# Kernel tuning notes

Measured on AMD Instinct MI355X. Metric: run time of the kernel, lower is better.

Reference implementation:

```python
import jax, jax.numpy as jnp
import numpy as np

EMB = 2048
HEADS = 16


def setup_inputs() -> dict:
    key = jax.random.key(0)
    k_x, k_wqkv, k_bqkv, k_wo, k_bo = jax.random.split(key, 5)
    B, S, E = 2, 2048, EMB
    x = jax.random.normal(k_x, (B, S, E), dtype=jnp.float32)
    # nn.Linear weights stored as (in, out) for x @ W + b convention
    W_qkv = jax.random.normal(k_wqkv, (E, 3 * E), dtype=jnp.float32) * 0.02
    b_qkv = jax.random.normal(k_bqkv, (3 * E,), dtype=jnp.float32) * 0.02
    W_out = jax.random.normal(k_wo, (E, E), dtype=jnp.float32) * 0.02
    b_out = jax.random.normal(k_bo, (E,), dtype=jnp.float32) * 0.02
    return {"x": x, "W_qkv": W_qkv, "b_qkv": b_qkv, "W_out": W_out, "b_out": b_out}


def reference(x, W_qkv, b_qkv, W_out, b_out):
    B, S, E = x.shape
    H = HEADS
    dh = E // H
    # QKV projection: (B,S,3E)
    qkv = x @ W_qkv + b_qkv
    # Faithful to torch: reshape (B,S,H,3*dh) THEN split -> interleaved per-head q/k/v
    qkv = qkv.reshape(B, S, H, 3 * dh).transpose(0, 2, 1, 3)  # (B,H,S,3*dh)
    q, k, v = jnp.split(qkv, 3, axis=-1)  # each (B,H,S,dh)
    q = q / jnp.asarray(dh, q.dtype) ** 0.5
    scores = jnp.einsum('bhqd,bhkd->bhqk', q, k)  # (B,H,S,S)
    weights = jax.nn.softmax(scores, axis=-1)
    attn = jnp.einsum('bhqk,bhkd->bhqd', weights, v)  # (B,H,S,dh)
    attn = attn.transpose(0, 2, 1, 3).reshape(B, S, E)
    return attn @ W_out + b_out
```

## Files before the change

kernel.cpp:

```cpp
#include <hip/hip_runtime.h>
#include <type_traits>
#include <utility>

#define DI __device__ __forceinline__

typedef unsigned short u16;
typedef float f32x4 __attribute__((ext_vector_type(4)));
typedef float f32x16 __attribute__((ext_vector_type(16)));
typedef short s16x8 __attribute__((ext_vector_type(8)));
typedef __bf16 bf16x8 __attribute__((ext_vector_type(8)));

template <typename V, typename = void>
struct mfma_ok : std::false_type {};
template <typename V>
struct mfma_ok<V, std::void_t<decltype(__builtin_amdgcn_mfma_f32_16x16x32_bf16(
    std::declval<V>(), std::declval<V>(), std::declval<f32x4>(), 0, 0, 0))>>
    : std::true_type {};
using frag_t = std::conditional_t<mfma_ok<bf16x8>::value, bf16x8, s16x8>;

union U128 {
  int4 i;
  frag_t f;
  u16 s[8];
};

DI f32x4 mfma16(const U128& a, const U128& b, f32x4 c) {
  return __builtin_amdgcn_mfma_f32_16x16x32_bf16(a.f, b.f, c, 0, 0, 0);
}
DI f32x16 mfma32(const U128& a, const U128& b, f32x16 c) {
  return __builtin_amdgcn_mfma_f32_32x32x16_bf16(a.f, b.f, c, 0, 0, 0);
}

DI u16 f2b(float x) {
  union { float f; unsigned u; } v; v.f = x;
  unsigned r = v.u + 0x7FFFu + ((v.u >> 16) & 1u);
  return (u16)(r >> 16);
}

#if __has_builtin(__builtin_amdgcn_exp2f)
#define EXP2F __builtin_amdgcn_exp2f
#else
#define EXP2F exp2f
#endif

typedef __attribute__((address_space(1))) void gas_t;
typedef __attribute__((address_space(3))) void las_t;
DI void gll16(const void* g, void* l) {
  __builtin_amdgcn_global_load_lds((gas_t*)g, (las_t*)l, 16, 0, 0);
}

__global__ __launch_bounds__(256) void k_conv_bf16(const float* __restrict__ in,
                                                   u16* __restrict__ out, int n4) {
  int i = blockIdx.x * 256 + threadIdx.x;
  if (i >= n4) return;
  float4 v = ((const float4*)in)[i];
  ushort4 o;
  o.x = f2b(v.x); o.y = f2b(v.y); o.z = f2b(v.z); o.w = f2b(v.w);
  ((ushort4*)out)[i] = o;
}

__global__ __launch_bounds__(256) void k_transpose_f2b(const float* __restrict__ in,
                                                       u16* __restrict__ out,
                                                       int R, int C) {
  __shared__ __attribute__((aligned(16))) u16 Tb[64][68];
  int t = threadIdx.x;
  long r0 = (long)blockIdx.y * 64, c0 = (long)blockIdx.x * 64;
  int cq = (t & 15) * 4, rr = t >> 4;
#pragma unroll
  for (int it = 0; it < 4; ++it) {
    int r = rr + it * 16;
    float4 v = *(const float4*)(in + (r0 + r) * C + c0 + cq);
    Tb[r][cq + 0] = f2b(v.x); Tb[r][cq + 1] = f2b(v.y);
    Tb[r][cq + 2] = f2b(v.z); Tb[r][cq + 3] = f2b(v.w);
  }
  __syncthreads();
#pragma unroll
  for (int it = 0; it < 2; ++it) {
    int ci = it * 256 + t;
    int cc = ci >> 3, ch = ci & 7, rb = ch * 8;
    unsigned p0 = Tb[rb + 0][cc] | ((unsigned)Tb[rb + 1][cc] << 16);
    unsigned p1 = Tb[rb + 2][cc] | ((unsigned)Tb[rb + 3][cc] << 16);
    unsigned p2 = Tb[rb + 4][cc] | ((unsigned)Tb[rb + 5][cc] << 16);
    unsigned p3 = Tb[rb + 6][cc] | ((unsigned)Tb[rb + 7][cc] << 16);
    *(int4*)(out + (c0 + cc) * R + r0 + rb) = make_int4(p0, p1, p2, p3);
  }
}

template <bool BF16OUT>
__global__ __launch_bounds__(256, 4) void k_gemm_bt(const u16* __restrict__ A,
                                                    const u16* __restrict__ Bt,
                                                    const float* __restrict__ bias,
                                                    void* __restrict__ Cout,
                                                    int M, int N, int K) {
  __shared__ __attribute__((aligned(16))) u16 As[128 * 64];
  __shared__ __attribute__((aligned(16))) u16 Bs[128 * 64];
  int t = threadIdx.x;
  int lane = t & 63, w = t >> 6, quad = lane >> 4, l15 = lane & 15;
  long m0 = (long)blockIdx.y * 128, n0 = (long)blockIdx.x * 128;
  int wr = (w >> 1) * 64, wc = (w & 1) * 64;
  int sw = l15 & 7;
  f32x4 acc[4][4] = {};
  for (int k0 = 0; k0 < K; k0 += 64) {
    __syncthreads();
#pragma unroll
    for (int it = 0; it < 4; ++it) {
      int ci = it * 256 + t;
      int row = ci >> 3, cl = (ci & 7) ^ (row & 7);
      gll16(A + (m0 + row) * K + k0 + cl * 8, As + ci * 8);
      gll16(Bt + (n0 + row) * K + k0 + cl * 8, Bs + ci * 8);
    }
    __syncthreads();
#pragma unroll
    for (int kk = 0; kk < 2; ++kk) {
      U128 a[4], b[4];
#pragma unroll
      for (int i = 0; i < 4; ++i)
        a[i].i = *(const int4*)(As + (wr + i * 16 + l15) * 64 + (((kk * 4 + quad) ^ sw) << 3));
#pragma unroll
      for (int j = 0; j < 4; ++j)
        b[j].i = *(const int4*)(Bs + (wc + j * 16 + l15) * 64 + (((kk * 4 + quad) ^ sw) << 3));
#pragma unroll
      for (int i = 0; i < 4; ++i)
#pragma unroll
        for (int j = 0; j < 4; ++j)
          acc[i][j] = mfma16(a[i], b[j], acc[i][j]);
    }
  }
  float bj[4];
#pragma unroll
  for (int j = 0; j < 4; ++j) bj[j] = bias[n0 + wc + j * 16 + l15];
#pragma unroll
  for (int i = 0; i < 4; ++i) {
#pragma unroll
    for (int r = 0; r < 4; ++r) {
      long row = m0 + wr + i * 16 + quad * 4 + r;
#pragma unroll
      for (int j = 0; j < 4; ++j) {
        long col = n0 + wc + j * 16 + l15;
        float v = acc[i][j][r] + bj[j];
        if (BF16OUT) {
          unsigned pb = f2b(v);
          unsigned other = __shfl_xor(pb, 1);
          if (!(l15 & 1))
            ((unsigned*)Cout)[(row * N + col) >> 1] = pb | (other << 16);
        } else {
          ((float*)Cout)[row * N + col] = v;
        }
      }
    }
  }
}

__global__ __launch_bounds__(256) void k_extract_kvt(const u16* __restrict__ qkv,
                                                     u16* __restrict__ kb,
                                                     u16* __restrict__ vt) {
  __shared__ __attribute__((aligned(16))) u16 Vb[64][136];
  int t = threadIdx.x;
  int s0 = blockIdx.x * 64;
  int bh = blockIdx.y, b = bh >> 4, h = bh & 15;
  long rowbase = (long)b * 2048 + s0;
  long krowout = (long)bh * 2048 + s0;
#pragma unroll
  for (int it = 0; it < 4; ++it) {
    int ci = it * 256 + t;
    int s = ci >> 4, ch = ci & 15;
    int4 v = *(const int4*)(qkv + (rowbase + s) * 6144 + h * 384 + 128 + ch * 8);
    *(int4*)(kb + (krowout + s) * 128 + ch * 8) = v;
  }
#pragma unroll
  for (int it = 0; it < 4; ++it) {
    int ci = it * 256 + t;
    int s = ci >> 4, ch = ci & 15;
    int4 v = *(const int4*)(qkv + (rowbase + s) * 6144 + h * 384 + 256 + ch * 8);
    *(int4*)(&Vb[s][ch * 8]) = v;
  }
  __syncthreads();
  long outbase = (long)bh * 128 * 2048 + s0;
#pragma unroll
  for (int it = 0; it < 4; ++it) {
    int ci = it * 256 + t;
    int d = ci >> 3, ch = ci & 7, sb = ch * 8;
    unsigned p0 = Vb[sb + 0][d] | ((unsigned)Vb[sb + 1][d] << 16);
    unsigned p1 = Vb[sb + 2][d] | ((unsigned)Vb[sb + 3][d] << 16);
    unsigned p2 = Vb[sb + 4][d] | ((unsigned)Vb[sb + 5][d] << 16);
    unsigned p3 = Vb[sb + 6][d] | ((unsigned)Vb[sb + 7][d] << 16);
    *(int4*)(vt + outbase + (long)d * 2048 + sb) = make_int4(p0, p1, p2, p3);
  }
}

__global__ __launch_bounds__(256, 2) void k_flash(const u16* __restrict__ qkv,
                                                  const u16* __restrict__ kb,
                                                  const u16* __restrict__ vt,
                                                  u16* __restrict__ attn) {
  __shared__ __attribute__((aligned(16))) u16 Ks[64 * 128];
  __shared__ __attribute__((aligned(16))) u16 Vts[128 * 64];
  int t = threadIdx.x;
  int lane = t & 63, w = t >> 6, l31 = lane & 31, h = lane >> 5;
  int q0 = blockIdx.x * 128 + w * 32;
  int bh = blockIdx.y, b = bh >> 4, hd = bh & 15;

  const u16* qbase = qkv + ((long)b * 2048 + q0 + l31) * 6144 + hd * 384;
  U128 qf[8];
#pragma unroll
  for (int dht = 0; dht < 8; ++dht)
    qf[dht].i = *(const int4*)(qbase + dht * 16 + h * 8);

  f32x16 O[4] = {};
  float lsum = 0.f;
  const float CEXP = 0.08838834764831845f * 1.4426950408889634f;
  const u16* kbh = kb + (long)bh * 2048 * 128;
  long vbase = (long)bh * 128 * 2048;

  for (int k0 = 0; k0 < 2048; k0 += 64) {
    __syncthreads();
#pragma unroll
    for (int it = 0; it < 4; ++it) {
      int ci = it * 256 + t;
      int key = ci >> 4, cp = ci & 15, cl = cp ^ (key & 7);
      gll16(kbh + (k0 + key) * 128 + cl * 8, Ks + ci * 8);
    }
#pragma unroll
    for (int it = 0; it < 4; ++it) {
      int ci = it * 256 + t;
      int d = ci >> 3, cp = ci & 7, cl = cp ^ (d & 7);
      gll16(vt + vbase + (long)d * 2048 + k0 + cl * 8, Vts + ci * 8);
    }
    __syncthreads();

    f32x16 St[2] = {};
#pragma unroll
    for (int kb2 = 0; kb2 < 2; ++kb2) {
      int row = kb2 * 32 + l31, sw = row & 7;
      const u16* kr = Ks + row * 128;
#pragma unroll
      for (int dht = 0; dht < 8; ++dht) {
        U128 kf;
        kf.i = *(const int4*)(kr + (((dht * 2 + h) ^ sw) << 3));
        St[kb2] = mfma32(kf, qf[dht], St[kb2]);
      }
    }

    float pk[2][16];
#pragma unroll
    for (int kb2 = 0; kb2 < 2; ++kb2)
#pragma unroll
      for (int r = 0; r < 16; ++r) {
        float p = EXP2F(St[kb2][r] * CEXP);
        pk[kb2][r] = p;
        lsum += p;
      }

    U128 pf[4];
#pragma unroll
    for (int kb2 = 0; kb2 < 2; ++kb2)
#pragma unroll
      for (int g = 0; g < 2; ++g) {
        float tmp[4], recv[4], lo[4], hi[4];
#pragma unroll
        for (int i = 0; i < 4; ++i)
          tmp[i] = h ? pk[kb2][g * 8 + i] : pk[kb2][g * 8 + 4 + i];
#pragma unroll
        for (int i = 0; i < 4; ++i) recv[i] = __shfl_xor(tmp[i], 32);
#pragma unroll
        for (int i = 0; i < 4; ++i) {
          lo[i] = h ? recv[i] : pk[kb2][g * 8 + i];
          hi[i] = h ? pk[kb2][g * 8 + 4 + i] : recv[i];
        }
        unsigned w0 = f2b(lo[0]) | ((unsigned)f2b(lo[1]) << 16);
        unsigned w1 = f2b(lo[2]) | ((unsigned)f2b(lo[3]) << 16);
        unsigned w2 = f2b(hi[0]) | ((unsigned)f2b(hi[1]) << 16);
        unsigned w3 = f2b(hi[2]) | ((unsigned)f2b(hi[3]) << 16);
        pf[kb2 * 2 + g].i = make_int4(w0, w1, w2, w3);
      }

#pragma unroll
    for (int kt = 0; kt < 4; ++kt)
#pragma unroll
      for (int dht = 0; dht < 4; ++dht) {
        int vrow = dht * 32 + l31, vsw = vrow & 7;
        U128 vf;
        vf.i = *(const int4*)(Vts + vrow * 64 + (((kt * 2 + h) ^ vsw) << 3));
        O[dht] = mfma32(vf, pf[kt], O[dht]);
      }
  }

  float ltot = lsum + __shfl_xor(lsum, 32);
  float inv = 1.f / ltot;
  long orow = (long)b * 2048 + q0 + l31;
  u16* ob = attn + orow * 2048 + hd * 128;
#pragma unroll
  for (int dht = 0; dht < 4; ++dht)
#pragma unroll
    for (int g = 0; g < 4; ++g) {
      int dh = dht * 32 + g * 8 + h * 4;
      float v0 = O[dht][4 * g + 0] * inv, v1 = O[dht][4 * g + 1] * inv;
      float v2 = O[dht][4 * g + 2] * inv, v3 = O[dht][4 * g + 3] * inv;
      uint2 pkd;
      pkd.x = f2b(v0) | ((unsigned)f2b(v1) << 16);
      pkd.y = f2b(v2) | ((unsigned)f2b(v3) << 16);
      *(uint2*)(ob + dh) = pkd;
    }
}

extern "C" void kernel_launch(void* const* d_in, const int* in_sizes, int n_in,
                              void* d_out, int out_size, void* d_ws, size_t ws_size,
                              hipStream_t stream) {
  const float* x    = (const float*)d_in[0];
  const float* Wqkv = (const float*)d_in[1];
  const float* bqkv = (const float*)d_in[2];
  const float* Wout = (const float*)d_in[3];
  const float* bout = (const float*)d_in[4];
  float* out = (float*)d_out;
  char* ws = (char*)d_ws;

  if (ws_size < 75497472u) return;

  u16* xb    = (u16*)d_out;
  u16* wqkvt = (u16*)(ws);
  u16* qkvb  = (u16*)(ws + 25165824);
  u16* vtb   = (u16*)d_out;
  u16* kbuf  = (u16*)((char*)d_out + 16777216);
  u16* woutt = (u16*)(ws);
  u16* attnb = (u16*)(ws + 8388608);

  k_conv_bf16<<<8192, 256, 0, stream>>>(x, xb, 2097152);
  k_transpose_f2b<<<dim3(96, 32), 256, 0, stream>>>(Wqkv, wqkvt, 2048, 6144);
  k_gemm_bt<true><<<dim3(48, 32), 256, 0, stream>>>(xb, wqkvt, bqkv, qkvb, 4096, 6144, 2048);
  k_extract_kvt<<<dim3(32, 32), 256, 0, stream>>>(qkvb, kbuf, vtb);
  k_transpose_f2b<<<dim3(32, 32), 256, 0, stream>>>(Wout, woutt, 2048, 2048);
  k_flash<<<dim3(16, 32), 256, 0, stream>>>(qkvb, kbuf, vtb, attnb);
  k_gemm_bt<false><<<dim3(16, 32), 256, 0, stream>>>(attnb, woutt, bout, out, 4096, 2048, 2048);
}
```

Before: 398.0 us.

## Split flash attention keys across warp pairs and vectorize fp32 GEMM stores

The flash kernel now gives each block 64 queries instead of 128. Each pair of warps handles half of the key range (split-K), and the partial outputs and row sums are combined through shared memory at the end. This doubles the grid to 1024 blocks and raises the occupancy hint to 3, to fill more CUs on a launch that was only 512 blocks. The cost is more K/V loads per query and an extra shared-memory reduction. Separately, the fp32 output GEMM epilogue pairs adjacent columns with a lane shuffle and writes them as 8-byte stores.

```diff
diff --git a/kernel.cpp b/kernel.cpp
--- a/kernel.cpp
+++ b/kernel.cpp
@@ -144,7 +144,12 @@
           if (!(l15 & 1))
             ((unsigned*)Cout)[(row * N + col) >> 1] = pb | (other << 16);
         } else {
-          ((float*)Cout)[row * N + col] = v;
+          unsigned bits = __float_as_uint(v);
+          unsigned other = __shfl_xor(bits, 1);
+          if (!(l15 & 1)) {
+            uint2 pr; pr.x = bits; pr.y = other;
+            *(uint2*)((float*)Cout + row * N + col) = pr;
+          }
         }
       }
     }
@@ -188,15 +193,20 @@
   }
 }
 
-__global__ __launch_bounds__(256, 2) void k_flash(const u16* __restrict__ qkv,
+__global__ __launch_bounds__(256, 3) void k_flash(const u16* __restrict__ qkv,
                                                   const u16* __restrict__ kb,
                                                   const u16* __restrict__ vt,
                                                   u16* __restrict__ attn) {
-  __shared__ __attribute__((aligned(16))) u16 Ks[64 * 128];
-  __shared__ __attribute__((aligned(16))) u16 Vts[128 * 64];
+  __shared__ __attribute__((aligned(16))) char smraw[49152];
+  u16* Ks = (u16*)smraw;
+  u16* Vts = (u16*)(smraw + 16384);
+  float* Om = (float*)smraw;
+  float* Lm = (float*)(smraw + 33024);
+
   int t = threadIdx.x;
   int lane = t & 63, w = t >> 6, l31 = lane & 31, h = lane >> 5;
-  int q0 = blockIdx.x * 128 + w * 32;
+  int qg = w & 1, kg = w >> 1, tl = t & 127;
+  int q0 = blockIdx.x * 64 + qg * 32;
   int bh = blockIdx.y, b = bh >> 4, hd = bh & 15;
 
   const u16* qbase = qkv + ((long)b * 2048 + q0 + l31) * 6144 + hd * 384;
@@ -210,96 +220,113 @@
   const float CEXP = 0.08838834764831845f * 1.4426950408889634f;
   const u16* kbh = kb + (long)bh * 2048 * 128;
   long vbase = (long)bh * 128 * 2048;
-
-  for (int k0 = 0; k0 < 2048; k0 += 64) {
+  u16* KsH = Ks + kg * 4096;
+  u16* VtsH = Vts + kg * 8192;
+  int kstart = kg * 1024;
+  int sw15 = l31 & 15;
+
+  for (int tile = 0; tile < 32; ++tile) {
+    int k0 = kstart + tile * 32;
     __syncthreads();
 #pragma unroll
     for (int it = 0; it < 4; ++it) {
-      int ci = it * 256 + t;
-      int key = ci >> 4, cp = ci & 15, cl = cp ^ (key & 7);
-      gll16(kbh + (k0 + key) * 128 + cl * 8, Ks + ci * 8);
-    }
-#pragma unroll
-    for (int it = 0; it < 4; ++it) {
-      int ci = it * 256 + t;
-      int d = ci >> 3, cp = ci & 7, cl = cp ^ (d & 7);
-      gll16(vt + vbase + (long)d * 2048 + k0 + cl * 8, Vts + ci * 8);
+      int ci = it * 128 + tl;
+      int key = ci >> 4, cp = ci & 15, cl = cp ^ (key & 15);
+      gll16(kbh + (long)(k0 + key) * 128 + cl * 8, KsH + ci * 8);
+    }
+    if (!(tile & 1)) {
+#pragma unroll
+      for (int it = 0; it < 8; ++it) {
+        int ci = it * 128 + tl;
+        int d = ci >> 3, cp = ci & 7, cl = cp ^ (d & 7);
+        gll16(vt + vbase + (long)d * 2048 + k0 + cl * 8, VtsH + ci * 8);
+      }
     }
     __syncthreads();
 
-    f32x16 St[2] = {};
-#pragma unroll
-    for (int kb2 = 0; kb2 < 2; ++kb2) {
-      int row = kb2 * 32 + l31, sw = row & 7;
-      const u16* kr = Ks + row * 128;
-#pragma unroll
-      for (int dht = 0; dht < 8; ++dht) {
-        U128 kf;
-        kf.i = *(const int4*)(kr + (((dht * 2 + h) ^ sw) << 3));
-        St[kb2] = mfma32(kf, qf[dht], St[kb2]);
-      }
-    }
-
-    float pk[2][16];
-#pragma unroll
-    for (int kb2 = 0; kb2 < 2; ++kb2)
+    f32x16 St = {};
+#pragma unroll
+    for (int dht = 0; dht < 8; ++dht) {
+      U128 kf;
+      kf.i = *(const int4*)(KsH + l31 * 128 + (((dht * 2 + h) ^ sw15) << 3));
+      St = mfma32(kf, qf[dht], St);
+    }
+
+    float pk[16];
+#pragma unroll
+    for (int r = 0; r < 16; ++r) {
+      float p = EXP2F(St[r] * CEXP);
+      pk[r] = p;
+      lsum += p;
+    }
+
+    U128 pf[2];
+#pragma unroll
+    for (int g = 0; g < 2; ++g) {
+      float tmp[4], recv[4], lo[4], hi[4];
+#pragma unroll
+      for (int i = 0; i < 4; ++i)
+        tmp[i] = h ? pk[g * 8 + i] : pk[g * 8 + 4 + i];
+#pragma unroll
+      for (int i = 0; i < 4; ++i) recv[i] = __shfl_xor(tmp[i], 32);
+#pragma unroll
+      for (int i = 0; i < 4; ++i) {
+        lo[i] = h ? recv[i] : pk[g * 8 + i];
+        hi[i] = h ? pk[g * 8 + 4 + i] : recv[i];
+      }
+      unsigned w0 = f2b(lo[0]) | ((unsigned)f2b(lo[1]) << 16);
+      unsigned w1 = f2b(lo[2]) | ((unsigned)f2b(lo[3]) << 16);
+      unsigned w2 = f2b(hi[0]) | ((unsigned)f2b(hi[1]) << 16);
+      unsigned w3 = f2b(hi[2]) | ((unsigned)f2b(hi[3]) << 16);
+      pf[g].i = make_int4(w0, w1, w2, w3);
+    }
+
+    int koff = (tile & 1) * 4;
+#pragma unroll
+    for (int kt = 0; kt < 2; ++kt)
+#pragma unroll
+      for (int dht = 0; dht < 4; ++dht) {
+        int vrow = dht * 32 + l31;
+        U128 vf;
+        vf.i = *(const int4*)(VtsH + vrow * 64 + (((koff + kt * 2 + h) ^ (vrow & 7)) << 3));
+        O[dht] = mfma32(vf, pf[kt], O[dht]);
+      }
+  }
+
+  float lhalf = lsum + __shfl_xor(lsum, 32);
+  __syncthreads();
+  if (kg == 1) {
+    if (lane < 32) Lm[qg * 32 + l31] = lhalf;
+#pragma unroll
+    for (int dht = 0; dht < 4; ++dht)
 #pragma unroll
       for (int r = 0; r < 16; ++r) {
-        float p = EXP2F(St[kb2][r] * CEXP);
-        pk[kb2][r] = p;
-        lsum += p;
-      }
-
-    U128 pf[4];
-#pragma unroll
-    for (int kb2 = 0; kb2 < 2; ++kb2)
-#pragma unroll
-      for (int g = 0; g < 2; ++g) {
-        float tmp[4], recv[4], lo[4], hi[4];
-#pragma unroll
-        for (int i = 0; i < 4; ++i)
-          tmp[i] = h ? pk[kb2][g * 8 + i] : pk[kb2][g * 8 + 4 + i];
-#pragma unroll
-        for (int i = 0; i < 4; ++i) recv[i] = __shfl_xor(tmp[i], 32);
-#pragma unroll
-        for (int i = 0; i < 4; ++i) {
-          lo[i] = h ? recv[i] : pk[kb2][g * 8 + i];
-          hi[i] = h ? pk[kb2][g * 8 + 4 + i] : recv[i];
-        }
-        unsigned w0 = f2b(lo[0]) | ((unsigned)f2b(lo[1]) << 16);
-        unsigned w1 = f2b(lo[2]) | ((unsigned)f2b(lo[3]) << 16);
-        unsigned w2 = f2b(hi[0]) | ((unsigned)f2b(hi[1]) << 16);
-        unsigned w3 = f2b(hi[2]) | ((unsigned)f2b(hi[3]) << 16);
-        pf[kb2 * 2 + g].i = make_int4(w0, w1, w2, w3);
-      }
-
-#pragma unroll
-    for (int kt = 0; kt < 4; ++kt)
-#pragma unroll
-      for (int dht = 0; dht < 4; ++dht) {
-        int vrow = dht * 32 + l31, vsw = vrow & 7;
-        U128 vf;
-        vf.i = *(const int4*)(Vts + vrow * 64 + (((kt * 2 + h) ^ vsw) << 3));
-        O[dht] = mfma32(vf, pf[kt], O[dht]);
-      }
-  }
-
-  float ltot = lsum + __shfl_xor(lsum, 32);
-  float inv = 1.f / ltot;
-  long orow = (long)b * 2048 + q0 + l31;
-  u16* ob = attn + orow * 2048 + hd * 128;
-#pragma unroll
-  for (int dht = 0; dht < 4; ++dht)
-#pragma unroll
-    for (int g = 0; g < 4; ++g) {
-      int dh = dht * 32 + g * 8 + h * 4;
-      float v0 = O[dht][4 * g + 0] * inv, v1 = O[dht][4 * g + 1] * inv;
-      float v2 = O[dht][4 * g + 2] * inv, v3 = O[dht][4 * g + 3] * inv;
-      uint2 pkd;
-      pkd.x = f2b(v0) | ((unsigned)f2b(v1) << 16);
-      pkd.y = f2b(v2) | ((unsigned)f2b(v3) << 16);
-      *(uint2*)(ob + dh) = pkd;
-    }
+        int dh = dht * 32 + (r & 3) + 8 * (r >> 2) + 4 * h;
+        Om[(qg * 32 + l31) * 129 + dh] = O[dht][r];
+      }
+  }
+  __syncthreads();
+  if (kg == 0) {
+    float ltot = lhalf + Lm[qg * 32 + l31];
+    float inv = 1.f / ltot;
+    long orow = (long)b * 2048 + q0 + l31;
+    u16* ob = attn + orow * 2048 + hd * 128;
+    const float* Oq = Om + (qg * 32 + l31) * 129;
+#pragma unroll
+    for (int dht = 0; dht < 4; ++dht)
+#pragma unroll
+      for (int g = 0; g < 4; ++g) {
+        int dh = dht * 32 + g * 8 + h * 4;
+        float v0 = (O[dht][4 * g + 0] + Oq[dh + 0]) * inv;
+        float v1 = (O[dht][4 * g + 1] + Oq[dh + 1]) * inv;
+        float v2 = (O[dht][4 * g + 2] + Oq[dh + 2]) * inv;
+        float v3 = (O[dht][4 * g + 3] + Oq[dh + 3]) * inv;
+        uint2 pkd;
+        pkd.x = f2b(v0) | ((unsigned)f2b(v1) << 16);
+        pkd.y = f2b(v2) | ((unsigned)f2b(v3) << 16);
+        *(uint2*)(ob + dh) = pkd;
+      }
+  }
 }
 
 extern "C" void kernel_launch(void* const* d_in, const int* in_sizes, int n_in,
@@ -328,6 +355,6 @@
   k_gemm_bt<true><<<dim3(48, 32), 256, 0, stream>>>(xb, wqkvt, bqkv, qkvb, 4096, 6144, 2048);
   k_extract_kvt<<<dim3(32, 32), 256, 0, stream>>>(qkvb, kbuf, vtb);
   k_transpose_f2b<<<dim3(32, 32), 256, 0, stream>>>(Wout, woutt, 2048, 2048);
-  k_flash<<<dim3(16, 32), 256, 0, stream>>>(qkvb, kbuf, vtb, attnb);
+  k_flash<<<dim3(32, 32), 256, 0, stream>>>(qkvb, kbuf, vtb, attnb);
   k_gemm_bt<false><<<dim3(16, 32), 256, 0, stream>>>(attnb, woutt, bout, out, 4096, 2048, 2048);
 }
```

Measured after the change: 437.4 us. 1.1x slower.

## Scatter QKV GEMM output directly into per-head Q/K/V buffers

Applied to the files above, without the earlier changes.

The QKV projection epilogue now writes each 128-column tile straight into head-major Q, K and V buffers instead of an interleaved (B,S,3E) array. The K copy in the extract kernel goes away, so it now only transposes V, and the flash kernel reads Q contiguously per head. The output GEMM's fp32 stores are also paired via a lane shuffle into 8-byte writes. This trades a copy pass and strided Q loads for a slightly more complex scatter epilogue and more workspace.

```diff
diff --git a/kernel.cpp b/kernel.cpp
--- a/kernel.cpp
+++ b/kernel.cpp
@@ -86,11 +86,14 @@
   }
 }
 
-template <bool BF16OUT>
+template <int MODE>
 __global__ __launch_bounds__(256, 4) void k_gemm_bt(const u16* __restrict__ A,
                                                     const u16* __restrict__ Bt,
                                                     const float* __restrict__ bias,
                                                     void* __restrict__ Cout,
+                                                    u16* __restrict__ qb,
+                                                    u16* __restrict__ kbv,
+                                                    u16* __restrict__ vb,
                                                     int M, int N, int K) {
   __shared__ __attribute__((aligned(16))) u16 As[128 * 64];
   __shared__ __attribute__((aligned(16))) u16 Bs[128 * 64];
@@ -129,49 +132,53 @@
   float bj[4];
 #pragma unroll
   for (int j = 0; j < 4; ++j) bj[j] = bias[n0 + wc + j * 16 + l15];
+
+  int hidx = (int)(n0 / 384);
+  int rsel = (int)(n0 - hidx * 384) >> 7;
+  u16* route = (MODE == 1) ? (rsel == 0 ? qb : rsel == 1 ? kbv : vb) : nullptr;
+
 #pragma unroll
   for (int i = 0; i < 4; ++i) {
 #pragma unroll
-    for (int r = 0; r < 4; ++r) {
-      long row = m0 + wr + i * 16 + quad * 4 + r;
+    for (int rr2 = 0; rr2 < 4; ++rr2) {
+      long row = m0 + wr + i * 16 + quad * 4 + rr2;
 #pragma unroll
       for (int j = 0; j < 4; ++j) {
-        long col = n0 + wc + j * 16 + l15;
-        float v = acc[i][j][r] + bj[j];
-        if (BF16OUT) {
+        float v = acc[i][j][rr2] + bj[j];
+        if (MODE == 1) {
+          int bidx = (int)(row >> 11), s = (int)(row & 2047);
+          long obase = ((long)(bidx * 16 + hidx) * 2048 + s) * 128;
+          int dh = wc + j * 16 + l15;
           unsigned pb = f2b(v);
           unsigned other = __shfl_xor(pb, 1);
           if (!(l15 & 1))
-            ((unsigned*)Cout)[(row * N + col) >> 1] = pb | (other << 16);
+            ((unsigned*)route)[(obase + dh) >> 1] = pb | (other << 16);
         } else {
-          ((float*)Cout)[row * N + col] = v;
+          long col = n0 + wc + j * 16 + l15;
+          unsigned bits = __float_as_uint(v);
+          unsigned other = __shfl_xor(bits, 1);
+          if (!(l15 & 1)) {
+            uint2 pr; pr.x = bits; pr.y = other;
+            *(uint2*)((float*)Cout + row * N + col) = pr;
+          }
         }
       }
     }
   }
 }
 
-__global__ __launch_bounds__(256) void k_extract_kvt(const u16* __restrict__ qkv,
-                                                     u16* __restrict__ kb,
-                                                     u16* __restrict__ vt) {
+__global__ __launch_bounds__(256) void k_extract_vt(const u16* __restrict__ vb,
+                                                    u16* __restrict__ vt) {
   __shared__ __attribute__((aligned(16))) u16 Vb[64][136];
   int t = threadIdx.x;
   int s0 = blockIdx.x * 64;
-  int bh = blockIdx.y, b = bh >> 4, h = bh & 15;
-  long rowbase = (long)b * 2048 + s0;
-  long krowout = (long)bh * 2048 + s0;
+  int bh = blockIdx.y;
+  long inbase = ((long)bh * 2048 + s0) * 128;
 #pragma unroll
   for (int it = 0; it < 4; ++it) {
     int ci = it * 256 + t;
     int s = ci >> 4, ch = ci & 15;
-    int4 v = *(const int4*)(qkv + (rowbase + s) * 6144 + h * 384 + 128 + ch * 8);
-    *(int4*)(kb + (krowout + s) * 128 + ch * 8) = v;
-  }
-#pragma unroll
-  for (int it = 0; it < 4; ++it) {
-    int ci = it * 256 + t;
-    int s = ci >> 4, ch = ci & 15;
-    int4 v = *(const int4*)(qkv + (rowbase + s) * 6144 + h * 384 + 256 + ch * 8);
+    int4 v = *(const int4*)(vb + inbase + s * 128 + ch * 8);
     *(int4*)(&Vb[s][ch * 8]) = v;
   }
   __syncthreads();
@@ -188,7 +195,7 @@
   }
 }
 
-__global__ __launch_bounds__(256, 2) void k_flash(const u16* __restrict__ qkv,
+__global__ __launch_bounds__(256, 2) void k_flash(const u16* __restrict__ qb,
                                                   const u16* __restrict__ kb,
                                                   const u16* __restrict__ vt,
                                                   u16* __restrict__ attn) {
@@ -199,7 +206,7 @@
   int q0 = blockIdx.x * 128 + w * 32;
   int bh = blockIdx.y, b = bh >> 4, hd = bh & 15;
 
-  const u16* qbase = qkv + ((long)b * 2048 + q0 + l31) * 6144 + hd * 384;
+  const u16* qbase = qb + ((long)bh * 2048 + q0 + l31) * 128;
   U128 qf[8];
 #pragma unroll
   for (int dht = 0; dht < 8; ++dht)
@@ -217,7 +224,7 @@
     for (int it = 0; it < 4; ++it) {
       int ci = it * 256 + t;
       int key = ci >> 4, cp = ci & 15, cl = cp ^ (key & 7);
-      gll16(kbh + (k0 + key) * 128 + cl * 8, Ks + ci * 8);
+      gll16(kbh + (long)(k0 + key) * 128 + cl * 8, Ks + ci * 8);
     }
 #pragma unroll
     for (int it = 0; it < 4; ++it) {
@@ -317,17 +324,20 @@
 
   u16* xb    = (u16*)d_out;
   u16* wqkvt = (u16*)(ws);
-  u16* qkvb  = (u16*)(ws + 25165824);
+  u16* qbuf  = (u16*)(ws + 25165824);
+  u16* kbuf  = (u16*)(ws + 41943040);
+  u16* vbuf  = (u16*)(ws + 58720256);
   u16* vtb   = (u16*)d_out;
-  u16* kbuf  = (u16*)((char*)d_out + 16777216);
   u16* woutt = (u16*)(ws);
   u16* attnb = (u16*)(ws + 8388608);
 
   k_conv_bf16<<<8192, 256, 0, stream>>>(x, xb, 2097152);
   k_transpose_f2b<<<dim3(96, 32), 256, 0, stream>>>(Wqkv, wqkvt, 2048, 6144);
-  k_gemm_bt<true><<<dim3(48, 32), 256, 0, stream>>>(xb, wqkvt, bqkv, qkvb, 4096, 6144, 2048);
-  k_extract_kvt<<<dim3(32, 32), 256, 0, stream>>>(qkvb, kbuf, vtb);
+  k_gemm_bt<1><<<dim3(48, 32), 256, 0, stream>>>(xb, wqkvt, bqkv, nullptr,
+                                                 qbuf, kbuf, vbuf, 4096, 6144, 2048);
+  k_extract_vt<<<dim3(32, 32), 256, 0, stream>>>(vbuf, vtb);
   k_transpose_f2b<<<dim3(32, 32), 256, 0, stream>>>(Wout, woutt, 2048, 2048);
-  k_flash<<<dim3(16, 32), 256, 0, stream>>>(qkvb, kbuf, vtb, attnb);
-  k_gemm_bt<false><<<dim3(16, 32), 256, 0, stream>>>(attnb, woutt, bout, out, 4096, 2048, 2048);
-}
+  k_flash<<<dim3(16, 32), 256, 0, stream>>>(qbuf, kbuf, vtb, attnb);
+  k_gemm_bt<0><<<dim3(16, 32), 256, 0, stream>>>(attnb, woutt, bout, out,
+                                                 nullptr, nullptr, nullptr, 4096, 2048, 2048);
+}
```

Measured after the change: 397.4 us. Within noise of the previous version (-0.2%).
